# Performance work log

Measured on AMD Instinct MI355X. Metric: run time of the kernel, lower is better.

## Reference

```python
import jax, jax.numpy as jnp
import numpy as np

N = 50000          # nodes
E = 800000         # edges
F_IN = 64          # node_features (== LSTM hidden)
C = 100            # conv_out_channels of GatedGraphConv
T = 8              # n_target


def setup_inputs() -> dict:
    key = jax.random.key(0)
    ks = jax.random.split(key, 20)
    s = 0.05
    return {
        "x": jax.random.normal(ks[0], (N, F_IN), jnp.float32),
        "edge_index": jax.random.randint(ks[1], (2, E), 0, N, jnp.int64),
        "edge_weight": jax.random.uniform(ks[2], (E,), jnp.float32),
        "h_0": jax.random.normal(ks[3], (1, N, F_IN), jnp.float32),
        "c_0": jax.random.normal(ks[4], (1, N, F_IN), jnp.float32),
        # GatedGraphConv: weight [num_layers=1, C, C]
        "ggc_w": jax.random.normal(ks[5], (1, C, C), jnp.float32) * s,
        # GRUCell(C, C)
        "gru_w_ih": jax.random.normal(ks[6], (3 * C, C), jnp.float32) * s,
        "gru_w_hh": jax.random.normal(ks[7], (3 * C, C), jnp.float32) * s,
        "gru_b_ih": jnp.zeros((3 * C,), jnp.float32),
        "gru_b_hh": jnp.zeros((3 * C,), jnp.float32),
        # LSTM(input=C, hidden=F_IN, num_layers=1)
        "lstm_w_ih": jax.random.normal(ks[8], (4 * F_IN, C), jnp.float32) * s,
        "lstm_w_hh": jax.random.normal(ks[9], (4 * F_IN, F_IN), jnp.float32) * s,
        "lstm_b_ih": jnp.zeros((4 * F_IN,), jnp.float32),
        "lstm_b_hh": jnp.zeros((4 * F_IN,), jnp.float32),
        # final Linear(F_IN -> T)
        "lin_w": jax.random.normal(ks[10], (T, F_IN), jnp.float32) * s,
        "lin_b": jnp.zeros((T,), jnp.float32),
    }


def reference(x, edge_index, edge_weight, h_0, c_0,
              ggc_w, gru_w_ih, gru_w_hh, gru_b_ih, gru_b_hh,
              lstm_w_ih, lstm_w_hh, lstm_b_ih, lstm_b_hh, lin_w, lin_b):
    src, dst = edge_index[0], edge_index[1]
    # --- GatedGraphConv (1 layer, mean aggr) ---
    xp = jnp.pad(x, ((0, 0), (0, C - x.shape[1])))  # pad features to C
    m = xp @ ggc_w[0]                               # [N, C]
    msg = m[src] * edge_weight[:, None]             # [E, C] gather + weight
    summ = jax.ops.segment_sum(msg, dst, num_segments=N)
    cnt = jax.ops.segment_sum(jnp.ones_like(edge_weight), dst, num_segments=N)
    agg = summ / jnp.maximum(cnt, 1.0)[:, None]     # scatter-mean
    # GRUCell(agg, xp)
    gi = agg @ gru_w_ih.T + gru_b_ih
    gh = xp @ gru_w_hh.T + gru_b_hh
    i_r, i_z, i_n = jnp.split(gi, 3, axis=1)
    h_r, h_z, h_n = jnp.split(gh, 3, axis=1)
    r = jax.nn.sigmoid(i_r + h_r)
    z = jax.nn.sigmoid(i_z + h_z)
    n = jnp.tanh(i_n + r * h_n)
    conv_h = (1.0 - z) * n + z * xp                 # [N, C]
    # --- LSTM, one time step, batch=N, hidden=F_IN ---
    gates = conv_h @ lstm_w_ih.T + lstm_b_ih + h_0[0] @ lstm_w_hh.T + lstm_b_hh
    i_g, f_g, g_g, o_g = jnp.split(gates, 4, axis=1)
    i_g = jax.nn.sigmoid(i_g)
    f_g = jax.nn.sigmoid(f_g)
    g_g = jnp.tanh(g_g)
    o_g = jax.nn.sigmoid(o_g)
    c1 = f_g * c_0[0] + i_g * g_g                   # [N, F_IN]
    h1 = o_g * jnp.tanh(c1)                         # [N, F_IN]
    # --- relu + linear head ---
    out = jax.nn.relu(h1) @ lin_w.T + lin_b         # [N, T]
    return out, h1[None], c1[None]
```

## Files before the change

### kernel.cpp

```cpp
#include <hip/hip_runtime.h>

#define N_NODES 50000
#define N_EDGES 800000
#define F_INF   64
#define C_CH    100
#define T_OUT   8

typedef unsigned short u16;
typedef unsigned int   u32;
typedef __attribute__((ext_vector_type(8))) short bf16x8;
typedef __attribute__((ext_vector_type(4))) float f32x4;

__device__ __forceinline__ float sigmoidf_(float x) {
    return 1.0f / (1.0f + __expf(-x));
}
__device__ __forceinline__ float tanhf_(float x) {
    return 1.0f - 2.0f / (__expf(2.0f * x) + 1.0f);
}
__device__ __forceinline__ u16 f2bf(float f) {
    union { float f; u32 u; } v; v.f = f;
    u32 u = v.u;
    u += 0x7FFF + ((u >> 16) & 1);
    return (u16)(u >> 16);
}
__device__ __forceinline__ float bf2f(u16 h) {
    union { u32 u; float f; } v; v.u = ((u32)h) << 16;
    return v.f;
}
__device__ __forceinline__ float asf_(int i) {
    union { int i; float f; } v; v.i = i; return v.f;
}

#define XBF_B  1563
#define WGRU_ELEMS (4 * 128 * 128)
#define WL_ELEMS   (4 * 64 * 192)
#define WP_B  ((WGRU_ELEMS + WL_ELEMS + 255) / 256)
__global__ void k_prep(const float* __restrict__ x,
                       const float* __restrict__ ggc, const float* __restrict__ gwih,
                       const float* __restrict__ gwhh,
                       const float* __restrict__ lwih, const float* __restrict__ lwhh,
                       u16* __restrict__ xbf,
                       u16* __restrict__ Wgru, u16* __restrict__ Wl) {
    int gb = blockIdx.x;
    if (gb < XBF_B) {
        int idx = gb * 256 + threadIdx.x;
        if (idx >= N_NODES * F_INF / 8) return;
        float4 a = ((const float4*)x)[idx * 2];
        float4 b = ((const float4*)x)[idx * 2 + 1];
        uint4 p;
        p.x = (u32)f2bf(a.x) | ((u32)f2bf(a.y) << 16);
        p.y = (u32)f2bf(a.z) | ((u32)f2bf(a.w) << 16);
        p.z = (u32)f2bf(b.x) | ((u32)f2bf(b.y) << 16);
        p.w = (u32)f2bf(b.z) | ((u32)f2bf(b.w) << 16);
        ((uint4*)xbf)[idx] = p;
        return;
    }
    int idx = (gb - XBF_B) * 256 + threadIdx.x;
    if (idx < WGRU_ELEMS) {
        int g = idx >> 14;
        int r = idx & 16383;
        int c = r >> 7;
        int k = r & 127;
        float val = 0.0f;
        if (c < 100) {
            if (g < 3) {
                if (k < 64) {
                    const float* wr = gwih + (g * 100 + c) * 100;
                    const float* gr = ggc + k * 100;
                    float s = 0.0f;
#pragma unroll 4
                    for (int j = 0; j < 100; ++j) s += wr[j] * gr[j];
                    val = s;
                } else if (g < 2) {
                    val = gwhh[(g * 100 + c) * 100 + (k - 64)];
                }
            } else {
                if (k >= 64) val = gwhh[(200 + c) * 100 + (k - 64)];
            }
        }
        Wgru[idx] = f2bf(val);
    } else if (idx < WGRU_ELEMS + WL_ELEMS) {
        int i2 = idx - WGRU_ELEMS;
        int g = i2 / 12288;
        int r = i2 - g * 12288;
        int c = r / 192;
        int k = r - c * 192;
        int row = g * 64 + c;
        float val = 0.0f;
        if (k < 100) val = lwih[row * 100 + k];
        else if (k >= 128) val = lwhh[row * 64 + (k - 128)];
        Wl[i2] = f2bf(val);
    }
}

#define BK_NPB 64
#define BK_NB  ((N_NODES + BK_NPB - 1) / BK_NPB)
#define BCAP   1280
#define PART_T     1024
#define PART_CHUNK 8192
#define PART_B ((N_EDGES + PART_CHUNK - 1) / PART_CHUNK)
#define PART_LDS_SIZE 110880
__global__ __launch_bounds__(PART_T, 4) void k_part(const int* __restrict__ ei,
                                                    const float* __restrict__ ew,
                                                    int* __restrict__ bcur,
                                                    int2* __restrict__ bucket) {
    extern __shared__ __align__(16) char pls[];
    int2* se    = (int2*)pls;
    int*  gdst  = (int*)(pls + 65536);
    int*  hist  = (int*)(pls + 98304);
    int*  ebase = (int*)(pls + 101432);
    int*  cur   = (int*)(pls + 104560);
    int*  gbase = (int*)(pls + 107688);
    int*  wsum  = (int*)(pls + 110816);
    int tid = threadIdx.x;
    int e0 = blockIdx.x * PART_CHUNK;
    int cnt = N_EDGES - e0;
    if (cnt > PART_CHUNK) cnt = PART_CHUNK;

    for (int i = tid; i < BK_NB; i += PART_T) hist[i] = 0;
    __syncthreads();

    int srcr[8], dstr[8]; float wvr[8];
#pragma unroll
    for (int k = 0; k < 8; ++k) {
        int e = tid + k * PART_T;
        if (e < cnt) {
            srcr[k] = ei[e0 + e];
            dstr[k] = ei[N_EDGES + e0 + e];
            wvr[k]  = ew[e0 + e];
            atomicAdd(&hist[dstr[k] >> 6], 1);
        } else dstr[k] = -1;
    }
    __syncthreads();

    {
        int lane = tid & 63, w = tid >> 6;
        int h = (tid < BK_NB) ? hist[tid] : 0;
        int v = h;
#pragma unroll
        for (int off = 1; off < 64; off <<= 1) {
            int u = __shfl_up(v, off, 64);
            if (lane >= off) v += u;
        }
        if (lane == 63) wsum[w] = v;
        __syncthreads();
        if (tid < 16) {
            int s = wsum[tid];
#pragma unroll
            for (int off = 1; off < 16; off <<= 1) {
                int u = __shfl_up(s, off, 16);
                if (tid >= off) s += u;
            }
            wsum[tid] = s;
        }
        __syncthreads();
        if (tid < BK_NB) {
            int v2 = v + ((w > 0) ? wsum[w - 1] : 0);
            int ex = v2 - h;
            ebase[tid] = ex;
            cur[tid] = ex;
            gbase[tid] = (h > 0) ? atomicAdd(&bcur[tid * 16], h) : 0;
        }
    }
    __syncthreads();

#pragma unroll
    for (int k = 0; k < 8; ++k) {
        if (dstr[k] >= 0) {
            int b = dstr[k] >> 6;
            int p = atomicAdd(&cur[b], 1);
            int gl = gbase[b] + (p - ebase[b]);
            se[p] = make_int2(srcr[k] | ((dstr[k] & 63) << 16), __float_as_int(wvr[k]));
            gdst[p] = (gl < BCAP) ? (b * BCAP + gl) : -1;
        }
    }
    __syncthreads();

    for (int i = tid; i < cnt; i += PART_T) {
        int g = gdst[i];
        if (g >= 0) bucket[g] = se[i];
    }
}

__global__ __launch_bounds__(512, 3) void k_bagg(
    const int2* __restrict__ bucket, const int* __restrict__ bcur,
    const u16* __restrict__ xbf, u16* __restrict__ xaggbf) {
    __shared__ int2 se[BCAP];
    __shared__ int  hist[64];
    __shared__ int  base[65];
    __shared__ int  cur[64];
    int tid = threadIdx.x;
    int b = blockIdx.x;
    int n0 = b * BK_NPB;

    if (tid < 64) hist[tid] = 0;
    __syncthreads();

    int cnt = bcur[b * 16];
    if (cnt > BCAP) cnt = BCAP;
    const int2* mybkt = bucket + (size_t)b * BCAP;

    int2 r0 = make_int2(0, 0), r1 = make_int2(0, 0), r2 = make_int2(0, 0);
    int nr = 0;
    if (tid < cnt)        { r0 = mybkt[tid];        atomicAdd(&hist[(r0.x >> 16) & 63], 1); nr = 1; }
    if (tid + 512 < cnt)  { r1 = mybkt[tid + 512];  atomicAdd(&hist[(r1.x >> 16) & 63], 1); nr = 2; }
    if (tid + 1024 < cnt) { r2 = mybkt[tid + 1024]; atomicAdd(&hist[(r2.x >> 16) & 63], 1); nr = 3; }
    __syncthreads();

    if (tid < 64) {
        int h = hist[tid];
        int v = h;
#pragma unroll
        for (int off = 1; off < 64; off <<= 1) {
            int u = __shfl_up(v, off, 64);
            if (tid >= off) v += u;
        }
        base[tid + 1] = v;
        if (tid == 0) base[0] = 0;
        cur[tid] = v - h;
    }
    __syncthreads();

    if (nr > 0) { int p = atomicAdd(&cur[(r0.x >> 16) & 63], 1); se[p] = r0; }
    if (nr > 1) { int p = atomicAdd(&cur[(r1.x >> 16) & 63], 1); se[p] = r1; }
    if (nr > 2) { int p = atomicAdd(&cur[(r2.x >> 16) & 63], 1); se[p] = r2; }
    __syncthreads();

    int w = tid >> 6, lane = tid & 63;
#pragma unroll
    for (int j = 0; j < 8; ++j) {
        int nl = w * 8 + j;
        int s = base[nl], epos = base[nl + 1];
        float acc = 0.0f;
        int i = s;
        for (; i + 3 < epos; i += 4) {
            int2 e0 = se[i], e1 = se[i + 1], e2 = se[i + 2], e3 = se[i + 3];
            float v0 = bf2f(xbf[(size_t)(e0.x & 0xFFFF) * 64 + lane]);
            float v1 = bf2f(xbf[(size_t)(e1.x & 0xFFFF) * 64 + lane]);
            float v2 = bf2f(xbf[(size_t)(e2.x & 0xFFFF) * 64 + lane]);
            float v3 = bf2f(xbf[(size_t)(e3.x & 0xFFFF) * 64 + lane]);
            acc += v0 * asf_(e0.y); acc += v1 * asf_(e1.y);
            acc += v2 * asf_(e2.y); acc += v3 * asf_(e3.y);
        }
        for (; i < epos; ++i) {
            int2 e0 = se[i];
            acc += bf2f(xbf[(size_t)(e0.x & 0xFFFF) * 64 + lane]) * asf_(e0.y);
        }
        int n = n0 + nl;
        if (n < N_NODES) {
            acc /= fmaxf((float)(epos - s), 1.0f);
            xaggbf[(size_t)n * 64 + lane] = f2bf(acc);
        }
    }
}

#define GRU_LDS_A1   136192
#define GRU_LDS_BIAS 155648
#define GRU_LDS_SIZE 158048
#define CONVH_LD     112
__global__ __launch_bounds__(1024, 4) void k_gru(
    const u16* __restrict__ xaggbf, const u16* __restrict__ xbf,
    const u16* __restrict__ Wgru,
    const float* __restrict__ gbih, const float* __restrict__ gbhh,
    u16* __restrict__ convh) {
    extern __shared__ __align__(16) char smem[];
    u16*   Wg   = (u16*)(smem);
    u16*   A1   = (u16*)(smem + GRU_LDS_A1);
    float* bias = (float*)(smem + GRU_LDS_BIAS);
    int tid = threadIdx.x;
    int n0 = blockIdx.x * 64;

#pragma unroll
    for (int i = 0; i < 8; ++i) {
        int idx = tid + i * 1024;
        int g = idx >> 11, rem = idx & 2047, row = rem >> 4, ch = rem & 15;
        if (row < 112) {
            uint4 v = ((const uint4*)Wgru)[idx];
            *(uint4*)(Wg + (g * 112 + row) * 152 + ch * 8) = v;
        }
    }
    {
        int row = tid >> 4, ch = tid & 15;
        int n = n0 + row;
        uint4 v = make_uint4(0, 0, 0, 0);
        if (n < N_NODES)
            v = (ch < 8) ? ((const uint4*)xaggbf)[n * 8 + ch]
                         : ((const uint4*)xbf)[n * 8 + (ch - 8)];
        *(uint4*)(A1 + row * 152 + ch * 8) = v;
    }
    if (tid < 600) bias[tid] = (tid < 300) ? gbih[tid] : gbhh[tid - 300];
    __syncthreads();

    int w = tid >> 6, lane = tid & 63, quad = lane >> 4, ln = lane & 15;
    int ct = w & 7, mh = w >> 3;
    if (ct >= 7) return;

    f32x4 ar[2], az[2], an[2], ah[2];
#pragma unroll
    for (int mt = 0; mt < 2; ++mt) {
        ar[mt] = (f32x4){0.f, 0.f, 0.f, 0.f};
        az[mt] = ar[mt]; an[mt] = ar[mt]; ah[mt] = ar[mt];
    }
    int rb = (ct * 16 + ln) * 152 + quad * 8;
#pragma unroll
    for (int kt = 0; kt < 4; ++kt) {
        bf16x8 b0 = *(const bf16x8*)(Wg + rb + kt * 32);
        bf16x8 b1 = *(const bf16x8*)(Wg + 17024 + rb + kt * 32);
        bf16x8 b2 = *(const bf16x8*)(Wg + 34048 + rb + kt * 32);
        bf16x8 b3 = *(const bf16x8*)(Wg + 51072 + rb + kt * 32);
#pragma unroll
        for (int mt = 0; mt < 2; ++mt) {
            bf16x8 a = *(const bf16x8*)(A1 + (mh * 32 + mt * 16 + ln) * 152 + kt * 32 + quad * 8);
            ar[mt] = __builtin_amdgcn_mfma_f32_16x16x32_bf16(a, b0, ar[mt], 0, 0, 0);
            az[mt] = __builtin_amdgcn_mfma_f32_16x16x32_bf16(a, b1, az[mt], 0, 0, 0);
            an[mt] = __builtin_amdgcn_mfma_f32_16x16x32_bf16(a, b2, an[mt], 0, 0, 0);
            ah[mt] = __builtin_amdgcn_mfma_f32_16x16x32_bf16(a, b3, ah[mt], 0, 0, 0);
        }
    }
    int c = ct * 16 + ln;
    float br = 0.f, bz = 0.f, bn2 = 0.f, bh2 = 0.f;
    if (c < 100) {
        br  = bias[c]       + bias[300 + c];
        bz  = bias[100 + c] + bias[400 + c];
        bn2 = bias[200 + c];
        bh2 = bias[500 + c];
    }
#pragma unroll
    for (int mt = 0; mt < 2; ++mt) {
#pragma unroll
        for (int reg = 0; reg < 4; ++reg) {
            int m = mh * 32 + mt * 16 + quad * 4 + reg;
            int n = n0 + m;
            float val = 0.0f;
            if (c < 100) {
                float rv = sigmoidf_(ar[mt][reg] + br);
                float zv = sigmoidf_(az[mt][reg] + bz);
                float nv = tanhf_(an[mt][reg] + bn2 + rv * (ah[mt][reg] + bh2));
                float xp = (c < F_INF) ? bf2f(A1[m * 152 + 64 + c]) : 0.0f;
                val = (1.0f - zv) * nv + zv * xp;
            }
            if (n < N_NODES) convh[(size_t)n * CONVH_LD + c] = f2bf(val);
        }
    }
}

#define LST_LDS_A2   110592
#define LST_LDS_BL   158976
#define LST_LDS_LWF  160000
#define LST_LDS_LBS  162048
#define LST_LDS_SIZE 162080
#define LST_TILE     112
__global__ __launch_bounds__(1024, 4) void k_lstm(
    const u16* __restrict__ convh, const float* __restrict__ h0,
    const float* __restrict__ c0, const u16* __restrict__ Wl,
    const float* __restrict__ lbih, const float* __restrict__ lbhh,
    const float* __restrict__ lw, const float* __restrict__ lb,
    float* __restrict__ out, float* __restrict__ h1, float* __restrict__ c1) {
    extern __shared__ __align__(16) char smem[];
    u16*   WlL = (u16*)(smem);
    u16*   A2  = (u16*)(smem + LST_LDS_A2);
    float* bl  = (float*)(smem + LST_LDS_BL);
    float* lwf = (float*)(smem + LST_LDS_LWF);
    float* lbs = (float*)(smem + LST_LDS_LBS);
    float* h1s = (float*)(smem + LST_LDS_A2);
    int tid = threadIdx.x;
    int n0 = blockIdx.x * LST_TILE;

#pragma unroll
    for (int i = 0; i < 6; ++i) {
        int idx = tid + i * 1024;
        int g = idx / 1536, rem = idx - g * 1536;
        int row = rem / 24, ch = rem - row * 24;
        uint4 v = ((const uint4*)Wl)[idx];
        *(uint4*)(WlL + (g * 64 + row) * 216 + ch * 8) = v;
    }
#pragma unroll
    for (int i = 0; i < 3; ++i) {
        int idx = tid + i * 1024;
        if (idx < 1568) {
            int row = idx / 14, ch = idx - row * 14;
            int n = n0 + row;
            uint4 v = make_uint4(0, 0, 0, 0);
            if (n < N_NODES) v = ((const uint4*)(convh))[(size_t)n * 14 + ch];
            *(uint4*)(A2 + row * 216 + ch * 8) = v;
        } else if (idx < 1792) {
            int j = idx - 1568;
            int row = j >> 1, ch2 = j & 1;
            *(uint4*)(A2 + row * 216 + 112 + ch2 * 8) = make_uint4(0, 0, 0, 0);
        } else if (idx < 2688) {
            int j = idx - 1792;
            int row = j >> 3, ch = j & 7;
            int n = n0 + row;
            uint4 p = make_uint4(0, 0, 0, 0);
            if (n < N_NODES) {
                float4 f0 = ((const float4*)h0)[n * 16 + ch * 2];
                float4 f1 = ((const float4*)h0)[n * 16 + ch * 2 + 1];
                p.x = (u32)f2bf(f0.x) | ((u32)f2bf(f0.y) << 16);
                p.y = (u32)f2bf(f0.z) | ((u32)f2bf(f0.w) << 16);
                p.z = (u32)f2bf(f1.x) | ((u32)f2bf(f1.y) << 16);
                p.w = (u32)f2bf(f1.z) | ((u32)f2bf(f1.w) << 16);
            }
            *(uint4*)(A2 + row * 216 + 128 + ch * 8) = p;
        }
    }
    if (tid < 256) bl[tid] = lbih[tid] + lbhh[tid];
    if (tid < 512) {
        int k = tid >> 3, t = tid & 7;
        lwf[tid] = lw[t * F_INF + k];
    }
    if (tid < 8) lbs[tid] = lb[tid];
    __syncthreads();

    int w = tid >> 6, lane = tid & 63, quad = lane >> 4, ln = lane & 15;
    int ct = w & 3, mgrp = w >> 2;
    int do_mt1 = (mgrp < 3);

    float h1v[2][4];
    {
        int c = ct * 16 + ln;
        float bi = bl[c], bff = bl[64 + c], bg = bl[128 + c], bo = bl[192 + c];
        f32x4 ai[2], af[2], ag[2], ao[2];
#pragma unroll
        for (int mt = 0; mt < 2; ++mt) {
            ai[mt] = (f32x4){0.f, 0.f, 0.f, 0.f};
            af[mt] = ai[mt]; ag[mt] = ai[mt]; ao[mt] = ai[mt];
        }
        int rb = (ct * 16 + ln) * 216 + quad * 8;
#pragma unroll
        for (int kt = 0; kt < 6; ++kt) {
            bf16x8 b0 = *(const bf16x8*)(WlL + rb + kt * 32);
            bf16x8 b1 = *(const bf16x8*)(WlL + 13824 + rb + kt * 32);
            bf16x8 b2 = *(const bf16x8*)(WlL + 27648 + rb + kt * 32);
            bf16x8 b3 = *(const bf16x8*)(WlL + 41472 + rb + kt * 32);
            bf16x8 a0 = *(const bf16x8*)(A2 + (mgrp * 32 + ln) * 216 + kt * 32 + quad * 8);
            ai[0] = __builtin_amdgcn_mfma_f32_16x16x32_bf16(a0, b0, ai[0], 0, 0, 0);
            af[0] = __builtin_amdgcn_mfma_f32_16x16x32_bf16(a0, b1, af[0], 0, 0, 0);
            ag[0] = __builtin_amdgcn_mfma_f32_16x16x32_bf16(a0, b2, ag[0], 0, 0, 0);
            ao[0] = __builtin_amdgcn_mfma_f32_16x16x32_bf16(a0, b3, ao[0], 0, 0, 0);
            if (do_mt1) {
                bf16x8 a1 = *(const bf16x8*)(A2 + (mgrp * 32 + 16 + ln) * 216 + kt * 32 + quad * 8);
                ai[1] = __builtin_amdgcn_mfma_f32_16x16x32_bf16(a1, b0, ai[1], 0, 0, 0);
                af[1] = __builtin_amdgcn_mfma_f32_16x16x32_bf16(a1, b1, af[1], 0, 0, 0);
                ag[1] = __builtin_amdgcn_mfma_f32_16x16x32_bf16(a1, b2, ag[1], 0, 0, 0);
                ao[1] = __builtin_amdgcn_mfma_f32_16x16x32_bf16(a1, b3, ao[1], 0, 0, 0);
            }
        }
#pragma unroll
        for (int mt = 0; mt < 2; ++mt) {
            if (mt == 1 && !do_mt1) break;
#pragma unroll
            for (int reg = 0; reg < 4; ++reg) {
                int m = mgrp * 32 + mt * 16 + quad * 4 + reg;
                int n = n0 + m;
                float iv = sigmoidf_(ai[mt][reg] + bi);
                float fv = sigmoidf_(af[mt][reg] + bff);
                float gv = tanhf_(ag[mt][reg] + bg);
                float ov = sigmoidf_(ao[mt][reg] + bo);
                float c0v = (n < N_NODES) ? c0[(size_t)n * F_INF + c] : 0.0f;
                float cc = fv * c0v + iv * gv;
                float hh = ov * tanhf_(cc);
                h1v[mt][reg] = hh;
                if (n < N_NODES) {
                    c1[(size_t)n * F_INF + c] = cc;
                    h1[(size_t)n * F_INF + c] = hh;
                }
            }
        }
    }
    __syncthreads();

    {
        int c = ct * 16 + ln;
#pragma unroll
        for (int mt = 0; mt < 2; ++mt) {
            if (mt == 1 && !do_mt1) break;
#pragma unroll
            for (int reg = 0; reg < 4; ++reg) {
                int m = mgrp * 32 + mt * 16 + quad * 4 + reg;
                h1s[m * 65 + c] = h1v[mt][reg];
            }
        }
    }
    __syncthreads();

    {
        int nl = tid & 127, t = tid >> 7;
        if (nl < LST_TILE) {
            float acc = lbs[t];
            const float* hr = h1s + nl * 65;
#pragma unroll 8
            for (int k = 0; k < F_INF; ++k)
                acc += fmaxf(hr[k], 0.0f) * lwf[k * 8 + t];
            int n = n0 + nl;
            if (n < N_NODES) out[(size_t)n * T_OUT + t] = acc;
        }
    }
}

extern "C" void kernel_launch(void* const* d_in, const int* in_sizes, int n_in,
                              void* d_out, int out_size, void* d_ws, size_t ws_size,
                              hipStream_t stream) {
    const float* x     = (const float*)d_in[0];
    const int*   ei    = (const int*)d_in[1];
    const float* ew    = (const float*)d_in[2];
    const float* h0    = (const float*)d_in[3];
    const float* c0    = (const float*)d_in[4];
    const float* ggc   = (const float*)d_in[5];
    const float* gwih  = (const float*)d_in[6];
    const float* gwhh  = (const float*)d_in[7];
    const float* gbih  = (const float*)d_in[8];
    const float* gbhh  = (const float*)d_in[9];
    const float* lwih  = (const float*)d_in[10];
    const float* lwhh  = (const float*)d_in[11];
    const float* lbih  = (const float*)d_in[12];
    const float* lbhh  = (const float*)d_in[13];
    const float* lw    = (const float*)d_in[14];
    const float* lb    = (const float*)d_in[15];

    float* out = (float*)d_out;
    float* h1  = out + (size_t)N_NODES * T_OUT;
    float* c1  = h1 + (size_t)N_NODES * F_INF;

    char* ws = (char*)d_ws;
    u16*   xaggbf = (u16*)ws;
    u16*   xbf    = (u16*)(ws + 6400000);
    u16*   Wgru   = (u16*)(ws + 12800000);
    u16*   Wl     = (u16*)(ws + 12931072);
    int2*  bucket = (int2*)(ws + 13029376);
    int*   bcur   = (int*)(ws + 21037056);
    u16*   convh  = (u16*)(ws + 13029376);

    static int lds_ok = 0;
    if (!lds_ok) {
        hipFuncSetAttribute((const void*)k_part,
                            hipFuncAttributeMaxDynamicSharedMemorySize, PART_LDS_SIZE);
        hipFuncSetAttribute((const void*)k_gru,
                            hipFuncAttributeMaxDynamicSharedMemorySize, GRU_LDS_SIZE);
        hipFuncSetAttribute((const void*)k_lstm,
                            hipFuncAttributeMaxDynamicSharedMemorySize, LST_LDS_SIZE);
        lds_ok = 1;
    }

    hipMemsetAsync(bcur, 0, BK_NB * 16 * sizeof(int), stream);

    k_prep<<<XBF_B + WP_B, 256, 0, stream>>>(
        x, ggc, gwih, gwhh, lwih, lwhh, xbf, Wgru, Wl);
    k_part<<<PART_B, PART_T, PART_LDS_SIZE, stream>>>(ei, ew, bcur, bucket);
    k_bagg<<<BK_NB, 512, 0, stream>>>(bucket, bcur, xbf, xaggbf);
    { int b = (N_NODES + 63) / 64;
      k_gru<<<b, 1024, GRU_LDS_SIZE, stream>>>(xaggbf, xbf, Wgru, gbih, gbhh, convh); }
    { int b = (N_NODES + LST_TILE - 1) / LST_TILE;
      k_lstm<<<b, 1024, LST_LDS_SIZE, stream>>>(convh, h0, c0, Wl,
                                                lbih, lbhh, lw, lb, out, h1, c1); }
}
```

Before: 215.7 us.

## Fuse GRU and LSTM kernels, keeping conv_h in LDS, with MFMA-fragment-packed weights

The separate GRU and LSTM kernels are merged into one 256-thread kernel per 64-node tile. conv_h now stays in shared memory instead of going out to global memory and back. Weights are pre-packed in k_prep into per-lane MFMA fragment order and loaded straight from global/L2 into registers, so the large per-block LDS weight copies are gone. This cuts LDS use and global traffic, in exchange for each block rereading the weights from cache and using more registers to hold them.

Measured after the change: 205.4 us. -4.8%, faster.

```diff
diff --git a/kernel.cpp b/kernel.cpp
--- a/kernel.cpp
+++ b/kernel.cpp
@@ -32,15 +32,15 @@
 }
 
 #define XBF_B  1563
-#define WGRU_ELEMS (4 * 128 * 128)
-#define WL_ELEMS   (4 * 64 * 192)
-#define WP_B  ((WGRU_ELEMS + WL_ELEMS + 255) / 256)
+#define WG2_ELEMS (7 * 4 * 4 * 64 * 8)
+#define WL2_ELEMS (4 * 6 * 4 * 64 * 8)
+#define WP_B  ((WG2_ELEMS + WL2_ELEMS + 255) / 256)
 __global__ void k_prep(const float* __restrict__ x,
                        const float* __restrict__ ggc, const float* __restrict__ gwih,
                        const float* __restrict__ gwhh,
                        const float* __restrict__ lwih, const float* __restrict__ lwhh,
                        u16* __restrict__ xbf,
-                       u16* __restrict__ Wgru, u16* __restrict__ Wl) {
+                       u16* __restrict__ Wg2, u16* __restrict__ Wl2) {
     int gb = blockIdx.x;
     if (gb < XBF_B) {
         int idx = gb * 256 + threadIdx.x;
@@ -56,11 +56,14 @@
         return;
     }
     int idx = (gb - XBF_B) * 256 + threadIdx.x;
-    if (idx < WGRU_ELEMS) {
-        int g = idx >> 14;
-        int r = idx & 16383;
-        int c = r >> 7;
-        int k = r & 127;
+    if (idx < WG2_ELEMS) {
+        int e    = idx & 7;
+        int lane = (idx >> 3) & 63;
+        int g    = (idx >> 9) & 3;
+        int kt   = (idx >> 11) & 3;
+        int ct   = idx >> 13;
+        int c = ct * 16 + (lane & 15);
+        int k = kt * 32 + (lane >> 4) * 8 + e;
         float val = 0.0f;
         if (c < 100) {
             if (g < 3) {
@@ -78,18 +81,20 @@
                 if (k >= 64) val = gwhh[(200 + c) * 100 + (k - 64)];
             }
         }
-        Wgru[idx] = f2bf(val);
-    } else if (idx < WGRU_ELEMS + WL_ELEMS) {
-        int i2 = idx - WGRU_ELEMS;
-        int g = i2 / 12288;
-        int r = i2 - g * 12288;
-        int c = r / 192;
-        int k = r - c * 192;
-        int row = g * 64 + c;
+        Wg2[idx] = f2bf(val);
+    } else if (idx < WG2_ELEMS + WL2_ELEMS) {
+        int i2 = idx - WG2_ELEMS;
+        int e    = i2 & 7;
+        int lane = (i2 >> 3) & 63;
+        int g    = (i2 >> 9) & 3;
+        int ctkt = i2 >> 11;
+        int ct = ctkt / 6, kt = ctkt - ct * 6;
+        int c = ct * 16 + (lane & 15);
+        int k = kt * 32 + (lane >> 4) * 8 + e;
         float val = 0.0f;
-        if (k < 100) val = lwih[row * 100 + k];
-        else if (k >= 128) val = lwhh[row * 64 + (k - 128)];
-        Wl[i2] = f2bf(val);
+        if (k < 100) val = lwih[(g * 64 + c) * 100 + k];
+        else if (k >= 128) val = lwhh[(g * 64 + c) * 64 + (k - 128)];
+        Wl2[i2] = f2bf(val);
     }
 }
 
@@ -254,33 +259,32 @@
     }
 }
 
-#define GRU_LDS_A1   136192
-#define GRU_LDS_BIAS 155648
-#define GRU_LDS_SIZE 158048
-#define CONVH_LD     112
-__global__ __launch_bounds__(1024, 4) void k_gru(
+#define RNN_A2   19456
+#define RNN_BIAS 47104
+#define RNN_BL   49504
+#define RNN_LWF  50528
+#define RNN_LBS  52576
+__global__ __launch_bounds__(256, 3) void k_rnn(
     const u16* __restrict__ xaggbf, const u16* __restrict__ xbf,
-    const u16* __restrict__ Wgru,
+    const float* __restrict__ h0, const float* __restrict__ c0,
+    const u16* __restrict__ Wg2, const u16* __restrict__ Wl2,
     const float* __restrict__ gbih, const float* __restrict__ gbhh,
-    u16* __restrict__ convh) {
-    extern __shared__ __align__(16) char smem[];
-    u16*   Wg   = (u16*)(smem);
-    u16*   A1   = (u16*)(smem + GRU_LDS_A1);
-    float* bias = (float*)(smem + GRU_LDS_BIAS);
+    const float* __restrict__ lbih, const float* __restrict__ lbhh,
+    const float* __restrict__ lw, const float* __restrict__ lb,
+    float* __restrict__ out, float* __restrict__ h1, float* __restrict__ c1) {
+    __shared__ __align__(16) char smem[52608];
+    u16*   A1   = (u16*)(smem);
+    u16*   A2   = (u16*)(smem + RNN_A2);
+    float* bias = (float*)(smem + RNN_BIAS);
+    float* bl   = (float*)(smem + RNN_BL);
+    float* lwf  = (float*)(smem + RNN_LWF);
+    float* lbs  = (float*)(smem + RNN_LBS);
+    float* h1s  = (float*)(smem);
     int tid = threadIdx.x;
     int n0 = blockIdx.x * 64;
 
-#pragma unroll
-    for (int i = 0; i < 8; ++i) {
-        int idx = tid + i * 1024;
-        int g = idx >> 11, rem = idx & 2047, row = rem >> 4, ch = rem & 15;
-        if (row < 112) {
-            uint4 v = ((const uint4*)Wgru)[idx];
-            *(uint4*)(Wg + (g * 112 + row) * 152 + ch * 8) = v;
-        }
-    }
-    {
-        int row = tid >> 4, ch = tid & 15;
+    for (int i = tid; i < 1024; i += 256) {
+        int row = i >> 4, ch = i & 15;
         int n = n0 + row;
         uint4 v = make_uint4(0, 0, 0, 0);
         if (n < N_NODES)
@@ -288,181 +292,159 @@
                          : ((const uint4*)xbf)[n * 8 + (ch - 8)];
         *(uint4*)(A1 + row * 152 + ch * 8) = v;
     }
-    if (tid < 600) bias[tid] = (tid < 300) ? gbih[tid] : gbhh[tid - 300];
+    for (int i = tid; i < 512; i += 256) {
+        int row = i >> 3, ch = i & 7;
+        int n = n0 + row;
+        uint4 p = make_uint4(0, 0, 0, 0);
+        if (n < N_NODES) {
+            float4 f0 = ((const float4*)h0)[n * 16 + ch * 2];
+            float4 f1 = ((const float4*)h0)[n * 16 + ch * 2 + 1];
+            p.x = (u32)f2bf(f0.x) | ((u32)f2bf(f0.y) << 16);
+            p.y = (u32)f2bf(f0.z) | ((u32)f2bf(f0.w) << 16);
+            p.z = (u32)f2bf(f1.x) | ((u32)f2bf(f1.y) << 16);
+            p.w = (u32)f2bf(f1.z) | ((u32)f2bf(f1.w) << 16);
+        }
+        *(uint4*)(A2 + row * 216 + 128 + ch * 8) = p;
+    }
+    for (int i = tid; i < 128; i += 256) {
+        int row = i >> 1, ch = i & 1;
+        *(uint4*)(A2 + row * 216 + 112 + ch * 8) = make_uint4(0, 0, 0, 0);
+    }
+    for (int i = tid; i < 600; i += 256)
+        bias[i] = (i < 300) ? gbih[i] : gbhh[i - 300];
+    if (tid < 256) bl[tid] = lbih[tid] + lbhh[tid];
+    for (int i = tid; i < 512; i += 256) {
+        int k = i >> 3, t = i & 7;
+        lwf[i] = lw[t * F_INF + k];
+    }
+    if (tid < 8) lbs[tid] = lb[tid];
     __syncthreads();
 
     int w = tid >> 6, lane = tid & 63, quad = lane >> 4, ln = lane & 15;
-    int ct = w & 7, mh = w >> 3;
-    if (ct >= 7) return;
-
-    f32x4 ar[2], az[2], an[2], ah[2];
-#pragma unroll
-    for (int mt = 0; mt < 2; ++mt) {
-        ar[mt] = (f32x4){0.f, 0.f, 0.f, 0.f};
-        az[mt] = ar[mt]; an[mt] = ar[mt]; ah[mt] = ar[mt];
-    }
-    int rb = (ct * 16 + ln) * 152 + quad * 8;
-#pragma unroll
-    for (int kt = 0; kt < 4; ++kt) {
-        bf16x8 b0 = *(const bf16x8*)(Wg + rb + kt * 32);
-        bf16x8 b1 = *(const bf16x8*)(Wg + 17024 + rb + kt * 32);
-        bf16x8 b2 = *(const bf16x8*)(Wg + 34048 + rb + kt * 32);
-        bf16x8 b3 = *(const bf16x8*)(Wg + 51072 + rb + kt * 32);
-#pragma unroll
-        for (int mt = 0; mt < 2; ++mt) {
-            bf16x8 a = *(const bf16x8*)(A1 + (mh * 32 + mt * 16 + ln) * 152 + kt * 32 + quad * 8);
-            ar[mt] = __builtin_amdgcn_mfma_f32_16x16x32_bf16(a, b0, ar[mt], 0, 0, 0);
-            az[mt] = __builtin_amdgcn_mfma_f32_16x16x32_bf16(a, b1, az[mt], 0, 0, 0);
-            an[mt] = __builtin_amdgcn_mfma_f32_16x16x32_bf16(a, b2, an[mt], 0, 0, 0);
-            ah[mt] = __builtin_amdgcn_mfma_f32_16x16x32_bf16(a, b3, ah[mt], 0, 0, 0);
-        }
-    }
-    int c = ct * 16 + ln;
-    float br = 0.f, bz = 0.f, bn2 = 0.f, bh2 = 0.f;
-    if (c < 100) {
-        br  = bias[c]       + bias[300 + c];
-        bz  = bias[100 + c] + bias[400 + c];
-        bn2 = bias[200 + c];
-        bh2 = bias[500 + c];
-    }
-#pragma unroll
-    for (int mt = 0; mt < 2; ++mt) {
-#pragma unroll
-        for (int reg = 0; reg < 4; ++reg) {
-            int m = mh * 32 + mt * 16 + quad * 4 + reg;
-            int n = n0 + m;
-            float val = 0.0f;
-            if (c < 100) {
-                float rv = sigmoidf_(ar[mt][reg] + br);
-                float zv = sigmoidf_(az[mt][reg] + bz);
-                float nv = tanhf_(an[mt][reg] + bn2 + rv * (ah[mt][reg] + bh2));
-                float xp = (c < F_INF) ? bf2f(A1[m * 152 + 64 + c]) : 0.0f;
-                val = (1.0f - zv) * nv + zv * xp;
-            }
-            if (n < N_NODES) convh[(size_t)n * CONVH_LD + c] = f2bf(val);
-        }
-    }
-}
-
-#define LST_LDS_A2   110592
-#define LST_LDS_BL   158976
-#define LST_LDS_LWF  160000
-#define LST_LDS_LBS  162048
-#define LST_LDS_SIZE 162080
-#define LST_TILE     112
-__global__ __launch_bounds__(1024, 4) void k_lstm(
-    const u16* __restrict__ convh, const float* __restrict__ h0,
-    const float* __restrict__ c0, const u16* __restrict__ Wl,
-    const float* __restrict__ lbih, const float* __restrict__ lbhh,
-    const float* __restrict__ lw, const float* __restrict__ lb,
-    float* __restrict__ out, float* __restrict__ h1, float* __restrict__ c1) {
-    extern __shared__ __align__(16) char smem[];
-    u16*   WlL = (u16*)(smem);
-    u16*   A2  = (u16*)(smem + LST_LDS_A2);
-    float* bl  = (float*)(smem + LST_LDS_BL);
-    float* lwf = (float*)(smem + LST_LDS_LWF);
-    float* lbs = (float*)(smem + LST_LDS_LBS);
-    float* h1s = (float*)(smem + LST_LDS_A2);
-    int tid = threadIdx.x;
-    int n0 = blockIdx.x * LST_TILE;
-
-#pragma unroll
-    for (int i = 0; i < 6; ++i) {
-        int idx = tid + i * 1024;
-        int g = idx / 1536, rem = idx - g * 1536;
-        int row = rem / 24, ch = rem - row * 24;
-        uint4 v = ((const uint4*)Wl)[idx];
-        *(uint4*)(WlL + (g * 64 + row) * 216 + ch * 8) = v;
-    }
-#pragma unroll
-    for (int i = 0; i < 3; ++i) {
-        int idx = tid + i * 1024;
-        if (idx < 1568) {
-            int row = idx / 14, ch = idx - row * 14;
-            int n = n0 + row;
-            uint4 v = make_uint4(0, 0, 0, 0);
-            if (n < N_NODES) v = ((const uint4*)(convh))[(size_t)n * 14 + ch];
-            *(uint4*)(A2 + row * 216 + ch * 8) = v;
-        } else if (idx < 1792) {
-            int j = idx - 1568;
-            int row = j >> 1, ch2 = j & 1;
-            *(uint4*)(A2 + row * 216 + 112 + ch2 * 8) = make_uint4(0, 0, 0, 0);
-        } else if (idx < 2688) {
-            int j = idx - 1792;
-            int row = j >> 3, ch = j & 7;
-            int n = n0 + row;
-            uint4 p = make_uint4(0, 0, 0, 0);
-            if (n < N_NODES) {
-                float4 f0 = ((const float4*)h0)[n * 16 + ch * 2];
-                float4 f1 = ((const float4*)h0)[n * 16 + ch * 2 + 1];
-                p.x = (u32)f2bf(f0.x) | ((u32)f2bf(f0.y) << 16);
-                p.y = (u32)f2bf(f0.z) | ((u32)f2bf(f0.w) << 16);
-                p.z = (u32)f2bf(f1.x) | ((u32)f2bf(f1.y) << 16);
-                p.w = (u32)f2bf(f1.z) | ((u32)f2bf(f1.w) << 16);
-            }
-            *(uint4*)(A2 + row * 216 + 128 + ch * 8) = p;
-        }
-    }
-    if (tid < 256) bl[tid] = lbih[tid] + lbhh[tid];
-    if (tid < 512) {
-        int k = tid >> 3, t = tid & 7;
-        lwf[tid] = lw[t * F_INF + k];
-    }
-    if (tid < 8) lbs[tid] = lb[tid];
-    __syncthreads();
-
-    int w = tid >> 6, lane = tid & 63, quad = lane >> 4, ln = lane & 15;
-    int ct = w & 3, mgrp = w >> 2;
-    int do_mt1 = (mgrp < 3);
-
-    float h1v[2][4];
+
+    for (int ct = w; ct < 7; ct += 4) {
+        bf16x8 wb[4][4];
+#pragma unroll
+        for (int kt = 0; kt < 4; ++kt)
+#pragma unroll
+            for (int g = 0; g < 4; ++g)
+                wb[kt][g] = ((const bf16x8*)Wg2)[((ct * 4 + kt) * 4 + g) * 64 + lane];
+        int c = ct * 16 + ln;
+        float br = 0.f, bz = 0.f, bn2 = 0.f, bh2 = 0.f;
+        if (c < 100) {
+            br  = bias[c]       + bias[300 + c];
+            bz  = bias[100 + c] + bias[400 + c];
+            bn2 = bias[200 + c];
+            bh2 = bias[500 + c];
+        }
+#pragma unroll
+        for (int mtp = 0; mtp < 2; ++mtp) {
+            f32x4 ar[2], az[2], an[2], ah[2];
+#pragma unroll
+            for (int mt = 0; mt < 2; ++mt) {
+                ar[mt] = (f32x4){0.f, 0.f, 0.f, 0.f};
+                az[mt] = ar[mt]; an[mt] = ar[mt]; ah[mt] = ar[mt];
+            }
+#pragma unroll
+            for (int kt = 0; kt < 4; ++kt) {
+#pragma unroll
+                for (int mt = 0; mt < 2; ++mt) {
+                    bf16x8 a = *(const bf16x8*)(A1 + (mtp * 32 + mt * 16 + ln) * 152 + kt * 32 + quad * 8);
+                    ar[mt] = __builtin_amdgcn_mfma_f32_16x16x32_bf16(a, wb[kt][0], ar[mt], 0, 0, 0);
+                    az[mt] = __builtin_amdgcn_mfma_f32_16x16x32_bf16(a, wb[kt][1], az[mt], 0, 0, 0);
+                    an[mt] = __builtin_amdgcn_mfma_f32_16x16x32_bf16(a, wb[kt][2], an[mt], 0, 0, 0);
+                    ah[mt] = __builtin_amdgcn_mfma_f32_16x16x32_bf16(a, wb[kt][3], ah[mt], 0, 0, 0);
+                }
+            }
+#pragma unroll
+            for (int mt = 0; mt < 2; ++mt) {
+#pragma unroll
+                for (int reg = 0; reg < 4; ++reg) {
+                    int m = mtp * 32 + mt * 16 + quad * 4 + reg;
+                    float val = 0.0f;
+                    if (c < 100) {
+                        float rv = sigmoidf_(ar[mt][reg] + br);
+                        float zv = sigmoidf_(az[mt][reg] + bz);
+                        float nv = tanhf_(an[mt][reg] + bn2 + rv * (ah[mt][reg] + bh2));
+                        float xp = (c < F_INF) ? bf2f(A1[m * 152 + 64 + c]) : 0.0f;
+                        val = (1.0f - zv) * nv + zv * xp;
+                    }
+                    A2[m * 216 + c] = f2bf(val);
+                }
+            }
+        }
+    }
+    __syncthreads();
+
+    float h1v[2][2][4];
     {
+        int ct = w;
         int c = ct * 16 + ln;
         float bi = bl[c], bff = bl[64 + c], bg = bl[128 + c], bo = bl[192 + c];
-        f32x4 ai[2], af[2], ag[2], ao[2];
-#pragma unroll
-        for (int mt = 0; mt < 2; ++mt) {
-            ai[mt] = (f32x4){0.f, 0.f, 0.f, 0.f};
-            af[mt] = ai[mt]; ag[mt] = ai[mt]; ao[mt] = ai[mt];
-        }
-        int rb = (ct * 16 + ln) * 216 + quad * 8;
-#pragma unroll
-        for (int kt = 0; kt < 6; ++kt) {
-            bf16x8 b0 = *(const bf16x8*)(WlL + rb + kt * 32);
-            bf16x8 b1 = *(const bf16x8*)(WlL + 13824 + rb + kt * 32);
-            bf16x8 b2 = *(const bf16x8*)(WlL + 27648 + rb + kt * 32);
-            bf16x8 b3 = *(const bf16x8*)(WlL + 41472 + rb + kt * 32);
-            bf16x8 a0 = *(const bf16x8*)(A2 + (mgrp * 32 + ln) * 216 + kt * 32 + quad * 8);
-            ai[0] = __builtin_amdgcn_mfma_f32_16x16x32_bf16(a0, b0, ai[0], 0, 0, 0);
-            af[0] = __builtin_amdgcn_mfma_f32_16x16x32_bf16(a0, b1, af[0], 0, 0, 0);
-            ag[0] = __builtin_amdgcn_mfma_f32_16x16x32_bf16(a0, b2, ag[0], 0, 0, 0);
-            ao[0] = __builtin_amdgcn_mfma_f32_16x16x32_bf16(a0, b3, ao[0], 0, 0, 0);
-            if (do_mt1) {
-                bf16x8 a1 = *(const bf16x8*)(A2 + (mgrp * 32 + 16 + ln) * 216 + kt * 32 + quad * 8);
-                ai[1] = __builtin_amdgcn_mfma_f32_16x16x32_bf16(a1, b0, ai[1], 0, 0, 0);
-                af[1] = __builtin_amdgcn_mfma_f32_16x16x32_bf16(a1, b1, af[1], 0, 0, 0);
-                ag[1] = __builtin_amdgcn_mfma_f32_16x16x32_bf16(a1, b2, ag[1], 0, 0, 0);
-                ao[1] = __builtin_amdgcn_mfma_f32_16x16x32_bf16(a1, b3, ao[1], 0, 0, 0);
-            }
-        }
-#pragma unroll
-        for (int mt = 0; mt < 2; ++mt) {
-            if (mt == 1 && !do_mt1) break;
-#pragma unroll
-            for (int reg = 0; reg < 4; ++reg) {
-                int m = mgrp * 32 + mt * 16 + quad * 4 + reg;
-                int n = n0 + m;
-                float iv = sigmoidf_(ai[mt][reg] + bi);
-                float fv = sigmoidf_(af[mt][reg] + bff);
-                float gv = tanhf_(ag[mt][reg] + bg);
-                float ov = sigmoidf_(ao[mt][reg] + bo);
-                float c0v = (n < N_NODES) ? c0[(size_t)n * F_INF + c] : 0.0f;
-                float cc = fv * c0v + iv * gv;
-                float hh = ov * tanhf_(cc);
-                h1v[mt][reg] = hh;
-                if (n < N_NODES) {
-                    c1[(size_t)n * F_INF + c] = cc;
-                    h1[(size_t)n * F_INF + c] = hh;
+#pragma unroll
+        for (int mtp = 0; mtp < 2; ++mtp) {
+            f32x4 ai[2], af[2], ag[2], ao[2];
+#pragma unroll
+            for (int mt = 0; mt < 2; ++mt) {
+                ai[mt] = (f32x4){0.f, 0.f, 0.f, 0.f};
+                af[mt] = ai[mt]; ag[mt] = ai[mt]; ao[mt] = ai[mt];
+            }
+            {
+                bf16x8 wbh[3][4];
+#pragma unroll
+                for (int kt = 0; kt < 3; ++kt)
+#pragma unroll
+                    for (int g = 0; g < 4; ++g)
+                        wbh[kt][g] = ((const bf16x8*)Wl2)[((ct * 6 + kt) * 4 + g) * 64 + lane];
+#pragma unroll
+                for (int kt = 0; kt < 3; ++kt) {
+#pragma unroll
+                    for (int mt = 0; mt < 2; ++mt) {
+                        bf16x8 a = *(const bf16x8*)(A2 + (mtp * 32 + mt * 16 + ln) * 216 + kt * 32 + quad * 8);
+                        ai[mt] = __builtin_amdgcn_mfma_f32_16x16x32_bf16(a, wbh[kt][0], ai[mt], 0, 0, 0);
+                        af[mt] = __builtin_amdgcn_mfma_f32_16x16x32_bf16(a, wbh[kt][1], af[mt], 0, 0, 0);
+                        ag[mt] = __builtin_amdgcn_mfma_f32_16x16x32_bf16(a, wbh[kt][2], ag[mt], 0, 0, 0);
+                        ao[mt] = __builtin_amdgcn_mfma_f32_16x16x32_bf16(a, wbh[kt][3], ao[mt], 0, 0, 0);
+                    }
+                }
+            }
+            {
+                bf16x8 wbh[3][4];
+#pragma unroll
+                for (int kt = 0; kt < 3; ++kt)
+#pragma unroll
+                    for (int g = 0; g < 4; ++g)
+                        wbh[kt][g] = ((const bf16x8*)Wl2)[((ct * 6 + kt + 3) * 4 + g) * 64 + lane];
+#pragma unroll
+                for (int kt = 0; kt < 3; ++kt) {
+#pragma unroll
+                    for (int mt = 0; mt < 2; ++mt) {
+                        bf16x8 a = *(const bf16x8*)(A2 + (mtp * 32 + mt * 16 + ln) * 216 + (kt + 3) * 32 + quad * 8);
+                        ai[mt] = __builtin_amdgcn_mfma_f32_16x16x32_bf16(a, wbh[kt][0], ai[mt], 0, 0, 0);
+                        af[mt] = __builtin_amdgcn_mfma_f32_16x16x32_bf16(a, wbh[kt][1], af[mt], 0, 0, 0);
+                        ag[mt] = __builtin_amdgcn_mfma_f32_16x16x32_bf16(a, wbh[kt][2], ag[mt], 0, 0, 0);
+                        ao[mt] = __builtin_amdgcn_mfma_f32_16x16x32_bf16(a, wbh[kt][3], ao[mt], 0, 0, 0);
+                    }
+                }
+            }
+#pragma unroll
+            for (int mt = 0; mt < 2; ++mt) {
+#pragma unroll
+                for (int reg = 0; reg < 4; ++reg) {
+                    int m = mtp * 32 + mt * 16 + quad * 4 + reg;
+                    int n = n0 + m;
+                    float iv = sigmoidf_(ai[mt][reg] + bi);
+                    float fv = sigmoidf_(af[mt][reg] + bff);
+                    float gv = tanhf_(ag[mt][reg] + bg);
+                    float ov = sigmoidf_(ao[mt][reg] + bo);
+                    float c0v = (n < N_NODES) ? c0[(size_t)n * F_INF + c] : 0.0f;
+                    float cc = fv * c0v + iv * gv;
+                    float hh = ov * tanhf_(cc);
+                    h1v[mtp][mt][reg] = hh;
+                    if (n < N_NODES) {
+                        c1[(size_t)n * F_INF + c] = cc;
+                        h1[(size_t)n * F_INF + c] = hh;
+                    }
                 }
             }
         }
@@ -470,30 +452,28 @@
     __syncthreads();
 
     {
-        int c = ct * 16 + ln;
-#pragma unroll
-        for (int mt = 0; mt < 2; ++mt) {
-            if (mt == 1 && !do_mt1) break;
-#pragma unroll
-            for (int reg = 0; reg < 4; ++reg) {
-                int m = mgrp * 32 + mt * 16 + quad * 4 + reg;
-                h1s[m * 65 + c] = h1v[mt][reg];
-            }
-        }
-    }
-    __syncthreads();
-
-    {
-        int nl = tid & 127, t = tid >> 7;
-        if (nl < LST_TILE) {
-            float acc = lbs[t];
-            const float* hr = h1s + nl * 65;
+        int c = w * 16 + ln;
+#pragma unroll
+        for (int mtp = 0; mtp < 2; ++mtp)
+#pragma unroll
+            for (int mt = 0; mt < 2; ++mt)
+#pragma unroll
+                for (int reg = 0; reg < 4; ++reg) {
+                    int m = mtp * 32 + mt * 16 + quad * 4 + reg;
+                    h1s[m * 65 + c] = h1v[mtp][mt][reg];
+                }
+    }
+    __syncthreads();
+
+    for (int o = tid; o < 512; o += 256) {
+        int nl = o & 63, t = o >> 6;
+        float acc = lbs[t];
+        const float* hr = h1s + nl * 65;
 #pragma unroll 8
-            for (int k = 0; k < F_INF; ++k)
-                acc += fmaxf(hr[k], 0.0f) * lwf[k * 8 + t];
-            int n = n0 + nl;
-            if (n < N_NODES) out[(size_t)n * T_OUT + t] = acc;
-        }
+        for (int k = 0; k < F_INF; ++k)
+            acc += fmaxf(hr[k], 0.0f) * lwf[k * 8 + t];
+        int n = n0 + nl;
+        if (n < N_NODES) out[(size_t)n * T_OUT + t] = acc;
     }
 }
 
@@ -524,32 +504,26 @@
     char* ws = (char*)d_ws;
     u16*   xaggbf = (u16*)ws;
     u16*   xbf    = (u16*)(ws + 6400000);
-    u16*   Wgru   = (u16*)(ws + 12800000);
-    u16*   Wl     = (u16*)(ws + 12931072);
-    int2*  bucket = (int2*)(ws + 13029376);
-    int*   bcur   = (int*)(ws + 21037056);
-    u16*   convh  = (u16*)(ws + 13029376);
+    u16*   Wg2    = (u16*)(ws + 12800000);
+    u16*   Wl2    = (u16*)(ws + 12914688);
+    int2*  bucket = (int2*)(ws + 13012992);
+    int*   bcur   = (int*)(ws + 21020672);
 
     static int lds_ok = 0;
     if (!lds_ok) {
         hipFuncSetAttribute((const void*)k_part,
                             hipFuncAttributeMaxDynamicSharedMemorySize, PART_LDS_SIZE);
-        hipFuncSetAttribute((const void*)k_gru,
-                            hipFuncAttributeMaxDynamicSharedMemorySize, GRU_LDS_SIZE);
-        hipFuncSetAttribute((const void*)k_lstm,
-                            hipFuncAttributeMaxDynamicSharedMemorySize, LST_LDS_SIZE);
         lds_ok = 1;
     }
 
     hipMemsetAsync(bcur, 0, BK_NB * 16 * sizeof(int), stream);
 
     k_prep<<<XBF_B + WP_B, 256, 0, stream>>>(
-        x, ggc, gwih, gwhh, lwih, lwhh, xbf, Wgru, Wl);
+        x, ggc, gwih, gwhh, lwih, lwhh, xbf, Wg2, Wl2);
     k_part<<<PART_B, PART_T, PART_LDS_SIZE, stream>>>(ei, ew, bcur, bucket);
     k_bagg<<<BK_NB, 512, 0, stream>>>(bucket, bcur, xbf, xaggbf);
     { int b = (N_NODES + 63) / 64;
-      k_gru<<<b, 1024, GRU_LDS_SIZE, stream>>>(xaggbf, xbf, Wgru, gbih, gbhh, convh); }
-    { int b = (N_NODES + LST_TILE - 1) / LST_TILE;
-      k_lstm<<<b, 1024, LST_LDS_SIZE, stream>>>(convh, h0, c0, Wl,
-                                                lbih, lbhh, lw, lb, out, h1, c1); }
-}
+      k_rnn<<<b, 256, 0, stream>>>(xaggbf, xbf, h0, c0, Wg2, Wl2,
+                                   gbih, gbhh, lbih, lbhh, lw, lb,
+                                   out, h1, c1); }
+}
```
